# Optimization experiments

Hardware: AMD Instinct MI355X
Metric: run time of the kernel (lower is better)

The kernel has to match this reference:

```python
import jax, jax.numpy as jnp
import numpy as np

B, NMAX, D, NUM = 1024, 128, 256, 4
EPS = 1e-8
NEG = -1e9


def segment_softmax(logits, seg):
    # torch_geometric-style softmax over ragged segments. logits: (T,)
    m = jax.ops.segment_max(logits, seg, num_segments=B)
    e = jnp.exp(logits - m[seg])
    s = jax.ops.segment_sum(e, seg, num_segments=B)
    return e / (s[seg] + 1e-16)


def to_dense(v, seg, pos):
    # scatter ragged rows into (B, NMAX, ...) dense batch
    return jnp.zeros((B, NMAX) + v.shape[1:], v.dtype).at[seg, pos].set(v)


def uot_badmm(x, q0d, maskf, a1, a2, a3, rho):
    # Bregman-ADMM solver for entropic unbalanced OT (f_method='badmm-e').
    # x: (B,N,D) cost (to be maximized); q0d, maskf: (B,N,1); a1,a2,a3,rho: (NUM,)
    log_p0 = jnp.full((B, 1, D), -jnp.log(float(D)), x.dtype)  # uniform dim prior
    log_q0 = jnp.log(q0d + EPS)                                # (B,N,1)
    log_t = log_q0 + log_p0                                    # T init = q0 p0^T
    log_s = log_t
    log_mu = log_p0
    log_eta = log_q0
    z = jnp.zeros_like(x)
    z1 = jnp.zeros_like(log_p0)
    z2 = jnp.zeros_like(log_q0)
    neg = (1.0 - maskf) * NEG  # exclude padded rows from N-axis softmax
    for k in range(NUM):
        r, b1, b2, b3 = rho[k], a1[k], a2[k], a3[k]
        # T-update: rows (over D) sum to eta
        y = (x - z + r * log_s) / (b2 + r)
        log_t = log_eta + jax.nn.log_softmax(y, axis=2)
        # S-update: columns (over N) sum to mu, masked
        y = (z + r * log_t) / (b1 + r) + neg
        log_s = log_mu + jax.nn.log_softmax(y, axis=1)
        # unbalanced marginal updates (KL to priors, weight a3)
        log_mu = (b3 * log_p0 - z1 + r * jax.nn.logsumexp(log_s, axis=1, keepdims=True)) / (b3 + r)
        log_eta = (b3 * log_q0 - z2 + r * jax.nn.logsumexp(log_t, axis=2, keepdims=True)) / (b3 + r)
        # dual ascent
        t = jnp.exp(log_t) * maskf
        s = jnp.exp(log_s) * maskf
        z = z + r * (t - s)
        z1 = z1 + r * (jnp.exp(log_mu) - jnp.sum(s, axis=1, keepdims=True))
        z2 = z2 + r * (jnp.exp(log_eta) - jnp.sum(t, axis=2, keepdims=True)) * maskf
    return jnp.exp(log_t) * maskf


def setup_inputs() -> dict:
    rng = np.random.default_rng(0)
    lengths = rng.integers(NMAX // 2, NMAX + 1, size=B)
    lengths[0] = NMAX  # ensure max size present
    batch = jnp.asarray(np.repeat(np.arange(B), lengths), dtype=jnp.int32)
    total = int(lengths.sum())
    ks = jax.random.split(jax.random.key(0), 8)
    x = jax.random.normal(ks[0], (total, D), jnp.float32)
    W1 = jax.random.normal(ks[1], (2 * D, D), jnp.float32) / np.float32(np.sqrt(D))
    W2 = jax.random.normal(ks[2], (1, 2 * D), jnp.float32) / np.float32(np.sqrt(2 * D))
    rho = 0.1 * jax.random.normal(ks[3], (NUM,), jnp.float32)
    a1 = 0.1 * jax.random.normal(ks[4], (NUM,), jnp.float32)
    a2 = 0.1 * jax.random.normal(ks[5], (NUM,), jnp.float32)
    a3 = 0.1 * jax.random.normal(ks[6], (NUM,), jnp.float32)
    return {"x": x, "batch": batch, "W1": W1, "W2": W2, "rho": rho, "a1": a1, "a2": a2, "a3": a3}


def reference(x, batch, W1, W2, rho, a1, a2, a3):
    # attention-based sample prior q0 (q0 != 'fixed' branch)
    h = jnp.tanh(x @ W1.T)          # (T, 2D)
    logits = (h @ W2.T)[:, 0]       # (T,)
    q0 = segment_softmax(logits, batch)[:, None]  # (T, 1)
    # ragged -> dense batch (to_dense_batch)
    counts = jax.ops.segment_sum(jnp.ones_like(batch), batch, num_segments=B)
    starts = jnp.cumsum(counts) - counts
    pos = jnp.arange(batch.shape[0]) - starts[batch]
    xd = to_dense(x, batch, pos)    # (B, NMAX, D)
    q0d = to_dense(q0, batch, pos)  # (B, NMAX, 1)
    mask = to_dense(jnp.ones((batch.shape[0], 1), x.dtype), batch, pos)  # (B, NMAX, 1)
    trans = uot_badmm(xd, q0d, mask,
                      jax.nn.softplus(a1), jax.nn.softplus(a2),
                      jax.nn.softplus(a3), jax.nn.softplus(rho))
    frot = D * xd * trans * mask    # (B, NMAX, D)
    return jnp.sum(frot, axis=1)    # (B, D)
```

## Files before the change

kernel.cpp:

```cpp
#include <hip/hip_runtime.h>
#include <math.h>

#define BB   1024
#define DD   256
#define LOGD 5.5451774444795624753f

typedef __attribute__((ext_vector_type(8))) short short8;
typedef __attribute__((ext_vector_type(4))) float f32x4;

__device__ __forceinline__ float wave_sum(float v){
  #pragma unroll
  for (int off=32; off>0; off>>=1) v += __shfl_xor(v, off, 64);
  return v;
}
__device__ __forceinline__ float wave_max(float v){
  #pragma unroll
  for (int off=32; off>0; off>>=1) v = fmaxf(v, __shfl_xor(v, off, 64));
  return v;
}
__device__ __forceinline__ float fast_tanh(float x){
  return 1.0f - 2.0f/(__expf(2.0f*x)+1.0f);
}
__device__ __forceinline__ unsigned short f2bf(float f){
  unsigned int u = __float_as_uint(f);
  unsigned int r = u + 0x7FFFu + ((u >> 16) & 1u);
  return (unsigned short)(r >> 16);
}

__global__ void k_pre(const float* __restrict__ W1, unsigned short* __restrict__ w1b,
                      const int* __restrict__ batch, int T, int* __restrict__ starts,
                      const float* __restrict__ rho, const float* __restrict__ a1,
                      const float* __restrict__ a2, const float* __restrict__ a3,
                      float* __restrict__ P)
{
  const int blk = blockIdx.x, tid = threadIdx.x;
  if (blk < 64){
    const int t = blk*256 + tid;
    #pragma unroll
    for (int i=0;i<2;i++){
      const int idx = (t*2 + i)*4;
      const float4 v = *(const float4*)(W1 + idx);
      *(ushort4*)(w1b + idx) = make_ushort4(f2bf(v.x), f2bf(v.y), f2bf(v.z), f2bf(v.w));
    }
  } else if (blk < 69){
    const int b = (blk-64)*256 + tid;
    if (b <= BB){
      int lo = 0, hi = T;
      while (lo < hi){ int mid = (lo+hi)>>1; if (batch[mid] < b) lo = mid+1; else hi = mid; }
      starts[b] = lo;
    }
  } else if (tid == 0){
    float lm = -LOGD, z1 = 0.f;
    for (int k=0;k<4;k++){
      float r  = log1pf(expf(rho[k]));
      float b1 = log1pf(expf(a1[k]));
      float b2 = log1pf(expf(a2[k]));
      float b3 = log1pf(expf(a3[k]));
      P[k]    = r;
      P[4+k]  = 1.f/(b1+r);
      P[8+k]  = 1.f/(b2+r);
      P[12+k] = lm;
      P[16+k] = b3;
      P[20+k] = 1.f/(b3+r);
      float lmn = (b3*(-LOGD) - z1 + r*lm)/(b3+r);
      z1 += r*(expf(lmn)-expf(lm));
      lm = lmn;
    }
  }
}

#define LPW 72
__global__ __launch_bounds__(512, 2) void k_mlp(
    const float* __restrict__ x, const unsigned short* __restrict__ w1b,
    const float* __restrict__ W2, float* __restrict__ logits, int T)
{
  __shared__ unsigned short Xs[128*LPW];
  __shared__ unsigned short Ws[128*LPW];
  __shared__ float lred[128];
  const int by = blockIdx.x;
  const int bx = blockIdx.y;
  const int tid = threadIdx.x;
  if (tid < 128) lred[tid] = 0.f;

  const int l = tid & 63;
  const int w = tid >> 6;
  const int wm = w >> 2;
  const int wn = w & 3;
  const int lr = l & 15, quad = l >> 4;
  const int srow = tid >> 2;
  const int sseg = tid & 3;
  const int wrow = tid >> 3;
  const int wseg = tid & 7;

  f32x4 acc[4][2];
  #pragma unroll
  for (int mi=0;mi<4;mi++)
    #pragma unroll
    for (int ni=0;ni<2;ni++) acc[mi][ni] = (f32x4){0.f,0.f,0.f,0.f};

  for (int kt=0; kt<4; kt++){
    const int k0 = kt*64;
    {
      const int grow = bx*128 + srow;
      #pragma unroll
      for (int i=0;i<4;i++){
        float4 v = make_float4(0.f,0.f,0.f,0.f);
        if (grow < T) v = *(const float4*)(x + (size_t)grow*DD + k0 + sseg*16 + i*4);
        *(ushort4*)&Xs[srow*LPW + sseg*16 + i*4] =
            make_ushort4(f2bf(v.x), f2bf(v.y), f2bf(v.z), f2bf(v.w));
      }
    }
    #pragma unroll
    for (int h=0; h<2; h++){
      const int r = h*64 + wrow;
      *(short8*)&Ws[r*LPW + wseg*8] =
          *(const short8*)(w1b + (size_t)(by*128 + r)*DD + k0 + wseg*8);
    }
    __syncthreads();
    #pragma unroll
    for (int ks=0; ks<2; ks++){
      short8 afr[4], bfr[2];
      #pragma unroll
      for (int mi=0;mi<4;mi++)
        afr[mi] = *(const short8*)&Xs[(wm*64 + mi*16 + lr)*LPW + ks*32 + quad*8];
      #pragma unroll
      for (int ni=0;ni<2;ni++)
        bfr[ni] = *(const short8*)&Ws[(wn*32 + ni*16 + lr)*LPW + ks*32 + quad*8];
      #pragma unroll
      for (int mi=0;mi<4;mi++)
        #pragma unroll
        for (int ni=0;ni<2;ni++)
          acc[mi][ni] = __builtin_amdgcn_mfma_f32_16x16x32_bf16(afr[mi], bfr[ni], acc[mi][ni], 0, 0, 0);
    }
    __syncthreads();
  }

  float w2v[2];
  #pragma unroll
  for (int ni=0;ni<2;ni++) w2v[ni] = W2[by*128 + wn*32 + ni*16 + lr];
  #pragma unroll
  for (int mi=0;mi<4;mi++){
    float p[4];
    #pragma unroll
    for (int v=0; v<4; v++){
      p[v] = fast_tanh(acc[mi][0][v])*w2v[0] + fast_tanh(acc[mi][1][v])*w2v[1];
      #pragma unroll
      for (int off=1; off<16; off<<=1) p[v] += __shfl_xor(p[v], off, 64);
    }
    if (lr == 0){
      #pragma unroll
      for (int v=0; v<4; v++)
        atomicAdd(&lred[wm*64 + mi*16 + quad*4 + v], p[v]);
    }
  }
  __syncthreads();
  if (tid < 128){
    const int grow = bx*128 + tid;
    if (grow < T) atomicAdd(logits + grow, lred[tid]);
  }
}

__global__ __launch_bounds__(1024, 4) void k_solver(
    const float* __restrict__ x, const float* __restrict__ logits,
    const int* __restrict__ starts, const float* __restrict__ P,
    float* __restrict__ out)
{
  __shared__ float A[128*DD];
  __shared__ float red[16*DD];
  __shared__ float colv[DD];
  const int b = blockIdx.x;
  const int start = starts[b];
  const int len = starts[b+1] - start;
  const int tid = threadIdx.x;
  const int w = tid >> 6, l = tid & 63;
  const int n0 = w*8;
  int nv = len - n0; nv = nv < 0 ? 0 : (nv > 8 ? 8 : nv);

  const float r0=P[0], r1=P[1], r2=P[2], r3=P[3];
  const float i10=P[4], i11=P[5], i12=P[6];
  const float i20=P[8], i21=P[9], i22=P[10], i23=P[11];
  const float mu0=P[12], mu1=P[13], mu2=P[14];
  const float b30=P[16], b31=P[17], b32=P[18];
  const float e30=P[20], e31=P[21], e32=P[22];

  const float* lg = logits + start;
  float v0 = (l      < len) ? lg[l]    : -3.0e38f;
  float v1 = (l+64   < len) ? lg[l+64] : -3.0e38f;
  float sm = wave_max(fmaxf(v0,v1));
  float se0 = (l    < len) ? __expf(v0-sm) : 0.f;
  float se1 = (l+64 < len) ? __expf(v1-sm) : 0.f;
  float ssum = wave_sum(se0+se1);
  const float sinv = 1.f/(ssum + 1e-16f);
  const float esel = (n0 < 64) ? se0 : se1;

  float lq[8], eta[8], z2r[8];
  float z[8][4];
  #pragma unroll
  for (int r=0;r<8;r++){
    const float ev = __shfl(esel, (n0+r)&63, 64);
    lq[r]  = __logf(ev*sinv + 1e-8f);
    eta[r] = lq[r];
    z2r[r] = 0.f;
    #pragma unroll
    for (int j=0;j<4;j++) z[r][j]=0.f;
  }

  {
    float sp[4] = {0.f,0.f,0.f,0.f};
    #pragma unroll
    for (int r=0;r<8;r++){
      if (r < nv){
        const float* xp = x + (size_t)(start+n0+r)*DD + l;
        const int base = (n0+r)*DD + l;
        const float a0 = lq[r] - LOGD;
        float xv[4], y[4];
        #pragma unroll
        for (int j=0;j<4;j++) xv[j] = xp[64*j];
        #pragma unroll
        for (int j=0;j<4;j++) y[j] = (xv[j] + r0*a0) * i20;
        float se = 0.f;
        #pragma unroll
        for (int j=0;j<4;j++) se += __expf(y[j]);
        se = wave_sum(se);
        const float off = eta[r] - __logf(se);
        #pragma unroll
        for (int j=0;j<4;j++){
          const float lt = off + y[j];
          A[base+64*j] = lt;
          sp[j] += __expf((r0*lt) * i10);
        }
        const float en = (b30*lq[r] - z2r[r] + r0*eta[r]) * e30;
        z2r[r] += r0*(__expf(en) - __expf(eta[r]));
        eta[r] = en;
      }
    }
    #pragma unroll
    for (int j=0;j<4;j++) red[w*DD + l + 64*j] = sp[j];
  }
  __syncthreads();
  if (tid < DD){
    float s = 0.f;
    #pragma unroll
    for (int ww=0; ww<16; ww++) s += red[ww*DD + tid];
    colv[tid] = __logf(s);
  }
  __syncthreads();

  #pragma unroll
  for (int k=1;k<3;k++){
    const float rkm = (k==1)? r0 : r1;
    const float ib1m= (k==1)? i10 : i11;
    const float mum = (k==1)? mu0 : mu1;
    const float rk  = (k==1)? r1 : r2;
    const float ib1k= (k==1)? i11 : i12;
    const float ib2k= (k==1)? i21 : i22;
    const float b3k = (k==1)? b31 : b32;
    const float e3k = (k==1)? e31 : e32;
    float lsc[4];
    #pragma unroll
    for (int j=0;j<4;j++) lsc[j] = colv[l+64*j];
    float sp[4] = {0.f,0.f,0.f,0.f};
    #pragma unroll
    for (int r=0;r<8;r++){
      if (r < nv){
        const float* xp = x + (size_t)(start+n0+r)*DD + l;
        const int base = (n0+r)*DD + l;
        float xv[4];
        #pragma unroll
        for (int j=0;j<4;j++) xv[j] = xp[64*j];
        float y[4], lsn[4];
        #pragma unroll
        for (int j=0;j<4;j++){
          const float lt  = A[base+64*j];
          const float ys  = (z[r][j] + rkm*lt) * ib1m;
          lsn[j] = mum + ys - lsc[j];
          z[r][j] += rkm*(__expf(lt) - __expf(lsn[j]));
          y[j] = (xv[j] - z[r][j] + rk*lsn[j]) * ib2k;
        }
        float se = 0.f;
        #pragma unroll
        for (int j=0;j<4;j++) se += __expf(y[j]);
        se = wave_sum(se);
        const float off = eta[r] - __logf(se);
        #pragma unroll
        for (int j=0;j<4;j++){
          const float lt = off + y[j];
          A[base+64*j] = lt;
          sp[j] += __expf((z[r][j] + rk*lt) * ib1k);
        }
        const float en = (b3k*lq[r] - z2r[r] + rk*eta[r]) * e3k;
        z2r[r] += rk*(__expf(en) - __expf(eta[r]));
        eta[r] = en;
      }
    }
    #pragma unroll
    for (int j=0;j<4;j++) red[w*DD + l + 64*j] = sp[j];
    __syncthreads();
    if (tid < DD){
      float s = 0.f;
      #pragma unroll
      for (int ww=0; ww<16; ww++) s += red[ww*DD + tid];
      colv[tid] = __logf(s);
    }
    __syncthreads();
  }

  {
    float lsc[4];
    #pragma unroll
    for (int j=0;j<4;j++) lsc[j] = colv[l+64*j];
    float op[4] = {0.f,0.f,0.f,0.f};
    #pragma unroll
    for (int r=0;r<8;r++){
      if (r < nv){
        const float* xp = x + (size_t)(start+n0+r)*DD + l;
        const int base = (n0+r)*DD + l;
        float xv[4];
        #pragma unroll
        for (int j=0;j<4;j++) xv[j] = xp[64*j];
        float y[4];
        #pragma unroll
        for (int j=0;j<4;j++){
          const float lt  = A[base+64*j];
          const float ys  = (z[r][j] + r2*lt) * i12;
          const float lsn = mu2 + ys - lsc[j];
          z[r][j] += r2*(__expf(lt) - __expf(lsn));
          y[j] = (xv[j] - z[r][j] + r3*lsn) * i23;
        }
        float ey[4], se = 0.f;
        #pragma unroll
        for (int j=0;j<4;j++){ ey[j] = __expf(y[j]); se += ey[j]; }
        se = wave_sum(se);
        const float rs = __expf(eta[r]) / se;
        #pragma unroll
        for (int j=0;j<4;j++) op[j] += xv[j]*ey[j]*rs;
      }
    }
    #pragma unroll
    for (int j=0;j<4;j++) red[w*DD + l + 64*j] = op[j];
    __syncthreads();
    if (tid < DD){
      float s = 0.f;
      #pragma unroll
      for (int ww=0; ww<16; ww++) s += red[ww*DD + tid];
      out[(size_t)b*DD + tid] = 256.0f * s;
    }
  }
}

extern "C" void kernel_launch(void* const* d_in, const int* in_sizes, int n_in,
                              void* d_out, int out_size, void* d_ws, size_t ws_size,
                              hipStream_t stream) {
  const float* x    = (const float*)d_in[0];
  const int*   batch= (const int*)d_in[1];
  const float* W1   = (const float*)d_in[2];
  const float* W2   = (const float*)d_in[3];
  const float* rho  = (const float*)d_in[4];
  const float* a1   = (const float*)d_in[5];
  const float* a2   = (const float*)d_in[6];
  const float* a3   = (const float*)d_in[7];
  float* out = (float*)d_out;
  const int T = in_sizes[1];

  float* logits = (float*)d_ws;
  int*   starts = (int*)(logits + T);
  float* P      = (float*)(starts + 1028);
  unsigned short* w1b = (unsigned short*)(P + 32);

  k_pre<<<70, 256, 0, stream>>>(W1, w1b, batch, T, starts, rho, a1, a2, a3, P);
  hipMemsetAsync(logits, 0, (size_t)T*sizeof(float), stream);
  k_mlp<<<dim3(4, (T+127)/128), 512, 0, stream>>>(x, w1b, W2, logits, T);
  k_solver<<<BB, 1024, 0, stream>>>(x, logits, starts, P, out);
}
```

Baseline: 358.6 us.

## Quantize log-transport plan in LDS to 16-bit fixed point to raise occupancy

Stores the per-block log-transport matrix in shared memory as 16-bit fixed-point values (scale 1/512, clamped at -63) instead of fp32, and drops the separate column buffer by reusing the reduction buffer. The shared-memory footprint shrinks, and launch bounds are raised so more blocks can be resident per CU. Per-row scalars are made wave-uniform with readfirstlane. Quantizing log T introduces an absolute error of about 0.001 in every value, which can accumulate across the ADMM iterations and change the results. Reusing the reduction buffer also needs an extra barrier per stage.

Measured after the change: 364.8 us. No clear change (+1.7%).

```diff
diff --git a/kernel.cpp b/kernel.cpp
--- a/kernel.cpp
+++ b/kernel.cpp
@@ -25,6 +25,15 @@
   unsigned int u = __float_as_uint(f);
   unsigned int r = u + 0x7FFFu + ((u >> 16) & 1u);
   return (unsigned short)(r >> 16);
+}
+__device__ __forceinline__ float rfl(float x){
+  return __uint_as_float(__builtin_amdgcn_readfirstlane(__float_as_uint(x)));
+}
+__device__ __forceinline__ int encq(float v){
+  return (int)(fmaxf(v, -63.0f)*512.0f - 0.5f);
+}
+__device__ __forceinline__ float decq(int q16){
+  return (float)q16 * (1.0f/512.0f);
 }
 
 __global__ void k_pre(const float* __restrict__ W1, unsigned short* __restrict__ w1b,
@@ -160,14 +169,13 @@
   }
 }
 
-__global__ __launch_bounds__(1024, 4) void k_solver(
+__global__ __launch_bounds__(1024, 8) void k_solver(
     const float* __restrict__ x, const float* __restrict__ logits,
     const int* __restrict__ starts, const float* __restrict__ P,
     float* __restrict__ out)
 {
-  __shared__ float A[128*DD];
+  __shared__ __align__(16) unsigned short As[128*DD];
   __shared__ float red[16*DD];
-  __shared__ float colv[DD];
   const int b = blockIdx.x;
   const int start = starts[b];
   const int len = starts[b+1] - start;
@@ -193,17 +201,19 @@
   const float sinv = 1.f/(ssum + 1e-16f);
   const float esel = (n0 < 64) ? se0 : se1;
 
-  float lq[8], eta[8], z2r[8];
+  float slq[8], eta[8], z2[8];
   float z[8][4];
   #pragma unroll
   for (int r=0;r<8;r++){
     const float ev = __shfl(esel, (n0+r)&63, 64);
-    lq[r]  = __logf(ev*sinv + 1e-8f);
-    eta[r] = lq[r];
-    z2r[r] = 0.f;
+    const float lqv = __logf(ev*sinv + 1e-8f);
+    slq[r] = rfl(lqv);
+    eta[r] = slq[r];
+    z2[r]  = 0.f;
     #pragma unroll
     for (int j=0;j<4;j++) z[r][j]=0.f;
   }
+  const int abase = (n0 << 8) + (l << 2);
 
   {
     float sp[4] = {0.f,0.f,0.f,0.f};
@@ -211,27 +221,28 @@
     for (int r=0;r<8;r++){
       if (r < nv){
         const float* xp = x + (size_t)(start+n0+r)*DD + l;
-        const int base = (n0+r)*DD + l;
-        const float a0 = lq[r] - LOGD;
+        const float a0 = slq[r] - LOGD;
         float xv[4], y[4];
         #pragma unroll
         for (int j=0;j<4;j++) xv[j] = xp[64*j];
-        #pragma unroll
-        for (int j=0;j<4;j++) y[j] = (xv[j] + r0*a0) * i20;
         float se = 0.f;
         #pragma unroll
-        for (int j=0;j<4;j++) se += __expf(y[j]);
+        for (int j=0;j<4;j++){ y[j] = (xv[j] + r0*a0) * i20; se += __expf(y[j]); }
         se = wave_sum(se);
         const float off = eta[r] - __logf(se);
-        #pragma unroll
-        for (int j=0;j<4;j++){
-          const float lt = off + y[j];
-          A[base+64*j] = lt;
-          sp[j] += __expf((r0*lt) * i10);
-        }
-        const float en = (b30*lq[r] - z2r[r] + r0*eta[r]) * e30;
-        z2r[r] += r0*(__expf(en) - __expf(eta[r]));
-        eta[r] = en;
+        int q[4];
+        #pragma unroll
+        for (int j=0;j<4;j++) q[j] = encq(off + y[j]);
+        uint2 pk;
+        pk.x = ((unsigned)q[0] & 0xffffu) | ((unsigned)q[1] << 16);
+        pk.y = ((unsigned)q[2] & 0xffffu) | ((unsigned)q[3] << 16);
+        *(uint2*)&As[abase + (r<<8)] = pk;
+        #pragma unroll
+        for (int j=0;j<4;j++) sp[j] += __expf((r0*decq(q[j])) * i10);
+        const float en = (b30*slq[r] - z2[r] + r0*eta[r]) * e30;
+        const float z2n = z2[r] + r0*(__expf(en) - __expf(eta[r]));
+        z2[r] = rfl(z2n);
+        eta[r] = rfl(en);
       }
     }
     #pragma unroll
@@ -242,7 +253,7 @@
     float s = 0.f;
     #pragma unroll
     for (int ww=0; ww<16; ww++) s += red[ww*DD + tid];
-    colv[tid] = __logf(s);
+    red[tid] = __logf(s);
   }
   __syncthreads();
 
@@ -258,39 +269,44 @@
     const float e3k = (k==1)? e31 : e32;
     float lsc[4];
     #pragma unroll
-    for (int j=0;j<4;j++) lsc[j] = colv[l+64*j];
+    for (int j=0;j<4;j++) lsc[j] = red[l+64*j];
+    __syncthreads();
     float sp[4] = {0.f,0.f,0.f,0.f};
     #pragma unroll
     for (int r=0;r<8;r++){
       if (r < nv){
         const float* xp = x + (size_t)(start+n0+r)*DD + l;
-        const int base = (n0+r)*DD + l;
         float xv[4];
         #pragma unroll
         for (int j=0;j<4;j++) xv[j] = xp[64*j];
-        float y[4], lsn[4];
+        const uint2 pk = *(const uint2*)&As[abase + (r<<8)];
+        float y[4], se = 0.f;
         #pragma unroll
         for (int j=0;j<4;j++){
-          const float lt  = A[base+64*j];
+          const int qv  = (j<2) ? (int)pk.x : (int)pk.y;
+          const int q16 = (j&1) ? (qv>>16) : ((qv<<16)>>16);
+          const float lt  = decq(q16);
           const float ys  = (z[r][j] + rkm*lt) * ib1m;
-          lsn[j] = mum + ys - lsc[j];
-          z[r][j] += rkm*(__expf(lt) - __expf(lsn[j]));
-          y[j] = (xv[j] - z[r][j] + rk*lsn[j]) * ib2k;
+          const float lsn = mum + ys - lsc[j];
+          z[r][j] += rkm*(__expf(lt) - __expf(lsn));
+          y[j] = (xv[j] - z[r][j] + rk*lsn) * ib2k;
+          se += __expf(y[j]);
         }
-        float se = 0.f;
-        #pragma unroll
-        for (int j=0;j<4;j++) se += __expf(y[j]);
         se = wave_sum(se);
         const float off = eta[r] - __logf(se);
-        #pragma unroll
-        for (int j=0;j<4;j++){
-          const float lt = off + y[j];
-          A[base+64*j] = lt;
-          sp[j] += __expf((z[r][j] + rk*lt) * ib1k);
-        }
-        const float en = (b3k*lq[r] - z2r[r] + rk*eta[r]) * e3k;
-        z2r[r] += rk*(__expf(en) - __expf(eta[r]));
-        eta[r] = en;
+        int q[4];
+        #pragma unroll
+        for (int j=0;j<4;j++) q[j] = encq(off + y[j]);
+        uint2 npk;
+        npk.x = ((unsigned)q[0] & 0xffffu) | ((unsigned)q[1] << 16);
+        npk.y = ((unsigned)q[2] & 0xffffu) | ((unsigned)q[3] << 16);
+        *(uint2*)&As[abase + (r<<8)] = npk;
+        #pragma unroll
+        for (int j=0;j<4;j++) sp[j] += __expf((z[r][j] + rk*decq(q[j])) * ib1k);
+        const float en = (b3k*slq[r] - z2[r] + rk*eta[r]) * e3k;
+        const float z2n = z2[r] + rk*(__expf(en) - __expf(eta[r]));
+        z2[r] = rfl(z2n);
+        eta[r] = rfl(en);
       }
     }
     #pragma unroll
@@ -300,7 +316,7 @@
       float s = 0.f;
       #pragma unroll
       for (int ww=0; ww<16; ww++) s += red[ww*DD + tid];
-      colv[tid] = __logf(s);
+      red[tid] = __logf(s);
     }
     __syncthreads();
   }
@@ -308,28 +324,30 @@
   {
     float lsc[4];
     #pragma unroll
-    for (int j=0;j<4;j++) lsc[j] = colv[l+64*j];
+    for (int j=0;j<4;j++) lsc[j] = red[l+64*j];
+    __syncthreads();
     float op[4] = {0.f,0.f,0.f,0.f};
     #pragma unroll
     for (int r=0;r<8;r++){
       if (r < nv){
         const float* xp = x + (size_t)(start+n0+r)*DD + l;
-        const int base = (n0+r)*DD + l;
         float xv[4];
         #pragma unroll
         for (int j=0;j<4;j++) xv[j] = xp[64*j];
-        float y[4];
+        const uint2 pk = *(const uint2*)&As[abase + (r<<8)];
+        float ey[4], se = 0.f;
         #pragma unroll
         for (int j=0;j<4;j++){
-          const float lt  = A[base+64*j];
+          const int qv  = (j<2) ? (int)pk.x : (int)pk.y;
+          const int q16 = (j&1) ? (qv>>16) : ((qv<<16)>>16);
+          const float lt  = decq(q16);
           const float ys  = (z[r][j] + r2*lt) * i12;
           const float lsn = mu2 + ys - lsc[j];
           z[r][j] += r2*(__expf(lt) - __expf(lsn));
-          y[j] = (xv[j] - z[r][j] + r3*lsn) * i23;
+          const float yv = (xv[j] - z[r][j] + r3*lsn) * i23;
+          ey[j] = __expf(yv);
+          se += ey[j];
         }
-        float ey[4], se = 0.f;
-        #pragma unroll
-        for (int j=0;j<4;j++){ ey[j] = __expf(y[j]); se += ey[j]; }
         se = wave_sum(se);
         const float rs = __expf(eta[r]) / se;
         #pragma unroll
```

## Keep solver state in registers as packed int16 and halve solver block size

Applied to the files above, without the earlier changes.

The solver no longer keeps the log-transport plan in a 128 KB shared-memory array. Each thread now holds its share of log_t and the dual z in registers, packed as 16-bit fixed-point pairs, and adds the row offset with a saturating packed-int16 add. Blocks drop to 512 threads, each wave handling 16 rows with float4 loads of x, and column partial sums are reduced through a padded 32-row shared buffer. The aim is to cut shared-memory traffic and the LDS footprint that limited occupancy. The cost is quantization error (1/512 for log_t, 1/4096 for z, with clamping), which could push results outside tolerance.

After: 352.4 us. Within noise of the previous version (-1.7%).

```diff
diff --git a/kernel.cpp b/kernel.cpp
--- a/kernel.cpp
+++ b/kernel.cpp
@@ -4,6 +4,7 @@
 #define BB   1024
 #define DD   256
 #define LOGD 5.5451774444795624753f
+#define RST  260
 
 typedef __attribute__((ext_vector_type(8))) short short8;
 typedef __attribute__((ext_vector_type(4))) float f32x4;
@@ -16,6 +17,13 @@
 __device__ __forceinline__ float wave_max(float v){
   #pragma unroll
   for (int off=32; off>0; off>>=1) v = fmaxf(v, __shfl_xor(v, off, 64));
+  return v;
+}
+__device__ __forceinline__ float grp_sum(float v){
+  v += __shfl_xor(v, 1, 64);
+  v += __shfl_xor(v, 2, 64);
+  v += __shfl_xor(v, 4, 64);
+  v += __shfl_xor(v, 8, 64);
   return v;
 }
 __device__ __forceinline__ float fast_tanh(float x){
@@ -25,6 +33,20 @@
   unsigned int u = __float_as_uint(f);
   unsigned int r = u + 0x7FFFu + ((u >> 16) & 1u);
   return (unsigned short)(r >> 16);
+}
+__device__ __forceinline__ float decq(int q16){ return (float)q16 * (1.0f/512.0f); }
+__device__ __forceinline__ int   zenc(float z){
+  float t = fmaf(z, 4096.0f, 12582912.0f);
+  return __float_as_int(t) - 0x4B400000;
+}
+__device__ __forceinline__ float zdec(int q){ return (float)q * (1.0f/4096.0f); }
+__device__ __forceinline__ int lo16(unsigned u){ return ((int)(u<<16))>>16; }
+__device__ __forceinline__ int hi16(unsigned u){ return ((int)u)>>16; }
+__device__ __forceinline__ unsigned pk2(int a, int b){
+  return ((unsigned)a & 0xffffu) | ((unsigned)b << 16);
+}
+__device__ __forceinline__ unsigned pkadd_sat(unsigned a, unsigned b){
+  unsigned d; asm("v_pk_add_i16 %0, %1, %2 clamp" : "=v"(d) : "v"(a), "v"(b)); return d;
 }
 
 __global__ void k_pre(const float* __restrict__ W1, unsigned short* __restrict__ w1b,
@@ -160,21 +182,22 @@
   }
 }
 
-__global__ __launch_bounds__(1024, 4) void k_solver(
+__global__ __launch_bounds__(512, 4) void k_solver(
     const float* __restrict__ x, const float* __restrict__ logits,
     const int* __restrict__ starts, const float* __restrict__ P,
     float* __restrict__ out)
 {
-  __shared__ float A[128*DD];
-  __shared__ float red[16*DD];
-  __shared__ float colv[DD];
+  __shared__ __align__(16) float red[32*RST];
+  __shared__ __align__(16) float colv[DD];
   const int b = blockIdx.x;
   const int start = starts[b];
   const int len = starts[b+1] - start;
   const int tid = threadIdx.x;
   const int w = tid >> 6, l = tid & 63;
-  const int n0 = w*8;
-  int nv = len - n0; nv = nv < 0 ? 0 : (nv > 8 ? 8 : nv);
+  const int sub = l >> 4;
+  const int c0  = l & 15;
+  const int n0 = w*16;
+  int nv = len - n0; nv = nv < 0 ? 0 : (nv > 16 ? 16 : nv);
 
   const float r0=P[0], r1=P[1], r2=P[2], r3=P[3];
   const float i10=P[4], i11=P[5], i12=P[6];
@@ -189,59 +212,78 @@
   float sm = wave_max(fmaxf(v0,v1));
   float se0 = (l    < len) ? __expf(v0-sm) : 0.f;
   float se1 = (l+64 < len) ? __expf(v1-sm) : 0.f;
-  float ssum = wave_sum(se0+se1);
-  const float sinv = 1.f/(ssum + 1e-16f);
+  float ssum0 = wave_sum(se0+se1);
+  const float sinv = 1.f/(ssum0 + 1e-16f);
   const float esel = (n0 < 64) ? se0 : se1;
 
-  float lq[8], eta[8], z2r[8];
-  float z[8][4];
-  #pragma unroll
-  for (int r=0;r<8;r++){
-    const float ev = __shfl(esel, (n0+r)&63, 64);
-    lq[r]  = __logf(ev*sinv + 1e-8f);
-    eta[r] = lq[r];
-    z2r[r] = 0.f;
-    #pragma unroll
-    for (int j=0;j<4;j++) z[r][j]=0.f;
-  }
+  float slqg[4], etag[4], z2g[4];
+  uint2 ap[4][4];
+  uint2 zp[4][4];
+  #pragma unroll
+  for (int g=0; g<4; g++){
+    const int row = n0 + 4*g + sub;
+    const float ev = __shfl(esel, row & 63, 64);
+    const float lq = __logf(ev*sinv + 1e-8f);
+    slqg[g] = lq; etag[g] = lq; z2g[g] = 0.f;
+    #pragma unroll
+    for (int q=0;q<4;q++){ zp[g][q].x = 0u; zp[g][q].y = 0u; }
+  }
+
+  const float* xbase = x + (size_t)(start + n0 + sub)*DD + 4*c0;
 
   {
-    float sp[4] = {0.f,0.f,0.f,0.f};
-    #pragma unroll
-    for (int r=0;r<8;r++){
-      if (r < nv){
-        const float* xp = x + (size_t)(start+n0+r)*DD + l;
-        const int base = (n0+r)*DD + l;
-        const float a0 = lq[r] - LOGD;
-        float xv[4], y[4];
-        #pragma unroll
-        for (int j=0;j<4;j++) xv[j] = xp[64*j];
-        #pragma unroll
-        for (int j=0;j<4;j++) y[j] = (xv[j] + r0*a0) * i20;
-        float se = 0.f;
-        #pragma unroll
-        for (int j=0;j<4;j++) se += __expf(y[j]);
-        se = wave_sum(se);
-        const float off = eta[r] - __logf(se);
-        #pragma unroll
-        for (int j=0;j<4;j++){
-          const float lt = off + y[j];
-          A[base+64*j] = lt;
-          sp[j] += __expf((r0*lt) * i10);
-        }
-        const float en = (b30*lq[r] - z2r[r] + r0*eta[r]) * e30;
-        z2r[r] += r0*(__expf(en) - __expf(eta[r]));
-        eta[r] = en;
+    float sp[16];
+    #pragma unroll
+    for (int j=0;j<16;j++) sp[j]=0.f;
+    #pragma unroll
+    for (int g=0; g<4; g++){
+      if (4*g + sub < nv){
+        const float* xp = xbase + (size_t)(4*g)*DD;
+        const float a0 = slqg[g] - LOGD;
+        float ss = 0.f;
+        #pragma unroll
+        for (int q=0;q<4;q++){
+          const float4 xv = *(const float4*)(xp + 64*q);
+          const float xvv[4] = {xv.x, xv.y, xv.z, xv.w};
+          int ny[4];
+          #pragma unroll
+          for (int j=0;j<4;j++){
+            const float y = (xvv[j] + r0*a0) * i20;
+            ss += __expf(y);
+            ny[j] = __float2int_rn(y*512.f);
+          }
+          ap[0][q] = ap[0][q];
+          ap[g][q].x = pk2(ny[0],ny[1]);
+          ap[g][q].y = pk2(ny[2],ny[3]);
+        }
+        ss = grp_sum(ss);
+        const float off = etag[g] - __logf(ss);
+        const int offi = __float2int_rn(fmaxf(off, -56.f)*512.f);
+        const unsigned offpk = pk2(offi, offi);
+        #pragma unroll
+        for (int q=0;q<4;q++){
+          ap[g][q].x = pkadd_sat(ap[g][q].x, offpk);
+          ap[g][q].y = pkadd_sat(ap[g][q].y, offpk);
+          sp[4*q+0] += __expf((r0*decq(lo16(ap[g][q].x))) * i10);
+          sp[4*q+1] += __expf((r0*decq(hi16(ap[g][q].x))) * i10);
+          sp[4*q+2] += __expf((r0*decq(lo16(ap[g][q].y))) * i10);
+          sp[4*q+3] += __expf((r0*decq(hi16(ap[g][q].y))) * i10);
+        }
+        const float en = (b30*slqg[g] - z2g[g] + r0*etag[g]) * e30;
+        z2g[g] += r0*(__expf(en) - __expf(etag[g]));
+        etag[g] = en;
       }
     }
     #pragma unroll
-    for (int j=0;j<4;j++) red[w*DD + l + 64*j] = sp[j];
+    for (int q=0;q<4;q++)
+      *(float4*)&red[(4*w+sub)*RST + 64*q + 4*c0] =
+          make_float4(sp[4*q], sp[4*q+1], sp[4*q+2], sp[4*q+3]);
   }
   __syncthreads();
   if (tid < DD){
     float s = 0.f;
     #pragma unroll
-    for (int ww=0; ww<16; ww++) s += red[ww*DD + tid];
+    for (int i=0;i<32;i++) s += red[i*RST + tid];
     colv[tid] = __logf(s);
   }
   __syncthreads();
@@ -256,93 +298,128 @@
     const float ib2k= (k==1)? i21 : i22;
     const float b3k = (k==1)? b31 : b32;
     const float e3k = (k==1)? e31 : e32;
-    float lsc[4];
-    #pragma unroll
-    for (int j=0;j<4;j++) lsc[j] = colv[l+64*j];
-    float sp[4] = {0.f,0.f,0.f,0.f};
-    #pragma unroll
-    for (int r=0;r<8;r++){
-      if (r < nv){
-        const float* xp = x + (size_t)(start+n0+r)*DD + l;
-        const int base = (n0+r)*DD + l;
-        float xv[4];
-        #pragma unroll
-        for (int j=0;j<4;j++) xv[j] = xp[64*j];
-        float y[4], lsn[4];
-        #pragma unroll
-        for (int j=0;j<4;j++){
-          const float lt  = A[base+64*j];
-          const float ys  = (z[r][j] + rkm*lt) * ib1m;
-          lsn[j] = mum + ys - lsc[j];
-          z[r][j] += rkm*(__expf(lt) - __expf(lsn[j]));
-          y[j] = (xv[j] - z[r][j] + rk*lsn[j]) * ib2k;
-        }
-        float se = 0.f;
-        #pragma unroll
-        for (int j=0;j<4;j++) se += __expf(y[j]);
-        se = wave_sum(se);
-        const float off = eta[r] - __logf(se);
-        #pragma unroll
-        for (int j=0;j<4;j++){
-          const float lt = off + y[j];
-          A[base+64*j] = lt;
-          sp[j] += __expf((z[r][j] + rk*lt) * ib1k);
-        }
-        const float en = (b3k*lq[r] - z2r[r] + rk*eta[r]) * e3k;
-        z2r[r] += rk*(__expf(en) - __expf(eta[r]));
-        eta[r] = en;
+    float sp[16];
+    #pragma unroll
+    for (int j=0;j<16;j++) sp[j]=0.f;
+    #pragma unroll
+    for (int g=0; g<4; g++){
+      if (4*g + sub < nv){
+        const float* xp = xbase + (size_t)(4*g)*DD;
+        float ss = 0.f;
+        #pragma unroll
+        for (int q=0;q<4;q++){
+          const float4 lscq = *(const float4*)&colv[64*q + 4*c0];
+          const float4 xv   = *(const float4*)(xp + 64*q);
+          const float xvv[4]  = {xv.x, xv.y, xv.z, xv.w};
+          const float lscv[4] = {lscq.x, lscq.y, lscq.z, lscq.w};
+          const int aq[4] = {lo16(ap[g][q].x), hi16(ap[g][q].x),
+                             lo16(ap[g][q].y), hi16(ap[g][q].y)};
+          const int zq[4] = {lo16(zp[g][q].x), hi16(zp[g][q].x),
+                             lo16(zp[g][q].y), hi16(zp[g][q].y)};
+          int ny[4], nz[4];
+          #pragma unroll
+          for (int j=0;j<4;j++){
+            const float lt = decq(aq[j]);
+            float zf = zdec(zq[j]);
+            const float ys  = (zf + rkm*lt) * ib1m;
+            const float lsn = mum + ys - lscv[j];
+            zf += rkm*(__expf(lt) - __expf(lsn));
+            nz[j] = zenc(zf);
+            const float y = (xvv[j] - zdec(nz[j]) + rk*lsn) * ib2k;
+            ss += __expf(y);
+            ny[j] = __float2int_rn(y*512.f);
+          }
+          ap[g][q].x = pk2(ny[0],ny[1]);
+          ap[g][q].y = pk2(ny[2],ny[3]);
+          zp[g][q].x = pk2(nz[0],nz[1]);
+          zp[g][q].y = pk2(nz[2],nz[3]);
+        }
+        ss = grp_sum(ss);
+        const float off = etag[g] - __logf(ss);
+        const int offi = __float2int_rn(fmaxf(off, -56.f)*512.f);
+        const unsigned offpk = pk2(offi, offi);
+        #pragma unroll
+        for (int q=0;q<4;q++){
+          ap[g][q].x = pkadd_sat(ap[g][q].x, offpk);
+          ap[g][q].y = pkadd_sat(ap[g][q].y, offpk);
+          sp[4*q+0] += __expf((zdec(lo16(zp[g][q].x)) + rk*decq(lo16(ap[g][q].x))) * ib1k);
+          sp[4*q+1] += __expf((zdec(hi16(zp[g][q].x)) + rk*decq(hi16(ap[g][q].x))) * ib1k);
+          sp[4*q+2] += __expf((zdec(lo16(zp[g][q].y)) + rk*decq(lo16(ap[g][q].y))) * ib1k);
+          sp[4*q+3] += __expf((zdec(hi16(zp[g][q].y)) + rk*decq(hi16(ap[g][q].y))) * ib1k);
+        }
+        const float en = (b3k*slqg[g] - z2g[g] + rk*etag[g]) * e3k;
+        z2g[g] += rk*(__expf(en) - __expf(etag[g]));
+        etag[g] = en;
       }
     }
     #pragma unroll
-    for (int j=0;j<4;j++) red[w*DD + l + 64*j] = sp[j];
+    for (int q=0;q<4;q++)
+      *(float4*)&red[(4*w+sub)*RST + 64*q + 4*c0] =
+          make_float4(sp[4*q], sp[4*q+1], sp[4*q+2], sp[4*q+3]);
     __syncthreads();
     if (tid < DD){
       float s = 0.f;
       #pragma unroll
-      for (int ww=0; ww<16; ww++) s += red[ww*DD + tid];
+      for (int i=0;i<32;i++) s += red[i*RST + tid];
       colv[tid] = __logf(s);
     }
     __syncthreads();
   }
 
   {
-    float lsc[4];
-    #pragma unroll
-    for (int j=0;j<4;j++) lsc[j] = colv[l+64*j];
-    float op[4] = {0.f,0.f,0.f,0.f};
-    #pragma unroll
-    for (int r=0;r<8;r++){
-      if (r < nv){
-        const float* xp = x + (size_t)(start+n0+r)*DD + l;
-        const int base = (n0+r)*DD + l;
-        float xv[4];
-        #pragma unroll
-        for (int j=0;j<4;j++) xv[j] = xp[64*j];
-        float y[4];
-        #pragma unroll
-        for (int j=0;j<4;j++){
-          const float lt  = A[base+64*j];
-          const float ys  = (z[r][j] + r2*lt) * i12;
-          const float lsn = mu2 + ys - lsc[j];
-          z[r][j] += r2*(__expf(lt) - __expf(lsn));
-          y[j] = (xv[j] - z[r][j] + r3*lsn) * i23;
-        }
-        float ey[4], se = 0.f;
-        #pragma unroll
-        for (int j=0;j<4;j++){ ey[j] = __expf(y[j]); se += ey[j]; }
-        se = wave_sum(se);
-        const float rs = __expf(eta[r]) / se;
-        #pragma unroll
-        for (int j=0;j<4;j++) op[j] += xv[j]*ey[j]*rs;
+    float op[16];
+    #pragma unroll
+    for (int j=0;j<16;j++) op[j]=0.f;
+    #pragma unroll
+    for (int g=0; g<4; g++){
+      if (4*g + sub < nv){
+        const float* xp = xbase + (size_t)(4*g)*DD;
+        float ey[16];
+        float ss = 0.f;
+        #pragma unroll
+        for (int q=0;q<4;q++){
+          const float4 lscq = *(const float4*)&colv[64*q + 4*c0];
+          const float4 xv   = *(const float4*)(xp + 64*q);
+          const float xvv[4]  = {xv.x, xv.y, xv.z, xv.w};
+          const float lscv[4] = {lscq.x, lscq.y, lscq.z, lscq.w};
+          const int aq[4] = {lo16(ap[g][q].x), hi16(ap[g][q].x),
+                             lo16(ap[g][q].y), hi16(ap[g][q].y)};
+          const int zq[4] = {lo16(zp[g][q].x), hi16(zp[g][q].x),
+                             lo16(zp[g][q].y), hi16(zp[g][q].y)};
+          #pragma unroll
+          for (int j=0;j<4;j++){
+            const float lt = decq(aq[j]);
+            float zf = zdec(zq[j]);
+            const float ys  = (zf + r2*lt) * i12;
+            const float lsn = mu2 + ys - lscv[j];
+            zf += r2*(__expf(lt) - __expf(lsn));
+            const float y = (xvv[j] - zf + r3*lsn) * i23;
+            const float e = __expf(y);
+            ey[4*q+j] = e;
+            ss += e;
+          }
+        }
+        ss = grp_sum(ss);
+        const float rs = __expf(etag[g]) / ss;
+        #pragma unroll
+        for (int q=0;q<4;q++){
+          const float4 xv = *(const float4*)(xp + 64*q);
+          op[4*q+0] += xv.x * ey[4*q+0] * rs;
+          op[4*q+1] += xv.y * ey[4*q+1] * rs;
+          op[4*q+2] += xv.z * ey[4*q+2] * rs;
+          op[4*q+3] += xv.w * ey[4*q+3] * rs;
+        }
       }
     }
     #pragma unroll
-    for (int j=0;j<4;j++) red[w*DD + l + 64*j] = op[j];
+    for (int q=0;q<4;q++)
+      *(float4*)&red[(4*w+sub)*RST + 64*q + 4*c0] =
+          make_float4(op[4*q], op[4*q+1], op[4*q+2], op[4*q+3]);
     __syncthreads();
     if (tid < DD){
       float s = 0.f;
       #pragma unroll
-      for (int ww=0; ww<16; ww++) s += red[ww*DD + tid];
+      for (int i=0;i<32;i++) s += red[i*RST + tid];
       out[(size_t)b*DD + tid] = 256.0f * s;
     }
   }
@@ -370,5 +447,5 @@
   k_pre<<<70, 256, 0, stream>>>(W1, w1b, batch, T, starts, rho, a1, a2, a3, P);
   hipMemsetAsync(logits, 0, (size_t)T*sizeof(float), stream);
   k_mlp<<<dim3(4, (T+127)/128), 512, 0, stream>>>(x, w1b, W2, logits, T);
-  k_solver<<<BB, 1024, 0, stream>>>(x, logits, starts, P, out);
-}
+  k_solver<<<BB, 512, 0, stream>>>(x, logits, starts, P, out);
+}
```
